# Performance work log

Measured on AMD Instinct MI355X. Metric: run time of the kernel, lower is better.

Reference implementation:

```python
import jax, jax.numpy as jnp
import numpy as np
from jax import lax

START, STOP, NTAGS = 18, 19, 20
NEG = -10000.0
V, E, H, L = 100000, 300, 512, 512  # vocab, embed_dim, per-direction hidden, seq_len


def setup_inputs() -> dict:
    key = jax.random.key(0)
    ks = jax.random.split(key, 16)
    f = lambda k, s: jax.random.normal(k, s, dtype=jnp.float32) * 0.05
    trans = jax.random.normal(ks[14], (NTAGS, NTAGS), dtype=jnp.float32)
    trans = trans.at[START, :].set(NEG).at[:, STOP].set(NEG)
    return {
        "sentence": jax.random.randint(ks[0], (L,), 0, V),
        "embed_table": f(ks[1], (V, E)),
        "w_ih_f": f(ks[2], (4 * H, E)), "w_hh_f": f(ks[3], (4 * H, H)),
        "b_ih_f": f(ks[4], (4 * H,)), "b_hh_f": f(ks[5], (4 * H,)),
        "w_ih_b": f(ks[6], (4 * H, E)), "w_hh_b": f(ks[7], (4 * H, H)),
        "b_ih_b": f(ks[8], (4 * H,)), "b_hh_b": f(ks[9], (4 * H,)),
        "h0": f(ks[10], (2, H)), "c0": f(ks[11], (2, H)),
        "w_out": f(ks[12], (NTAGS, 2 * H)), "b_out": f(ks[13], (NTAGS,)),
        "transitions": trans,
    }


def _lstm_dir(x, wih, whh, bih, bhh, h0, c0, reverse):
    # x: [L, E]; PyTorch gate order i, f, g, o
    b = bih + bhh
    def step(carry, xt):
        h, c = carry
        g = xt @ wih.T + h @ whh.T + b  # [4H]
        i, fg, gg, o = jnp.split(g, 4)
        c = jax.nn.sigmoid(fg) * c + jax.nn.sigmoid(i) * jnp.tanh(gg)
        h = jax.nn.sigmoid(o) * jnp.tanh(c)
        return (h, c), h
    _, hs = lax.scan(step, (h0, c0), x, reverse=reverse)
    return hs  # [L, H] in time order


def _lstm_feats(sentence, embed_table, w_ih_f, w_hh_f, b_ih_f, b_hh_f,
                w_ih_b, w_hh_b, b_ih_b, b_hh_b, h0, c0, w_out, b_out):
    x = embed_table[sentence]  # [L, E]
    hf = _lstm_dir(x, w_ih_f, w_hh_f, b_ih_f, b_hh_f, h0[0], c0[0], False)
    hb = _lstm_dir(x, w_ih_b, w_hh_b, b_ih_b, b_hh_b, h0[1], c0[1], True)
    h = jnp.concatenate([hf, hb], axis=-1)  # [L, 2H]
    return h @ w_out.T + b_out  # [L, NTAGS]


def reference(sentence, embed_table, w_ih_f, w_hh_f, b_ih_f, b_hh_f,
              w_ih_b, w_hh_b, b_ih_b, b_hh_b, h0, c0, w_out, b_out, transitions):
    feats = _lstm_feats(sentence, embed_table, w_ih_f, w_hh_f, b_ih_f, b_hh_f,
                        w_ih_b, w_hh_b, b_ih_b, b_hh_b, h0, c0, w_out, b_out)
    init = jnp.full((NTAGS,), NEG, dtype=feats.dtype).at[START].set(0.0)

    def vstep(fv, feat):
        scores = fv[None, :] + transitions  # [next_tag, prev_tag]
        bptr = jnp.argmax(scores, axis=1)
        return jnp.max(scores, axis=1) + feat, bptr

    fv, bptrs = lax.scan(vstep, init, feats)  # bptrs: [L, NTAGS]
    terminal = fv + transitions[STOP]
    best = jnp.argmax(terminal)

    def back(tag, bp):
        # tag is the best tag at step t; bp maps tag_t -> tag_{t-1}
        return bp[tag], tag

    _, path = lax.scan(back, best, bptrs, reverse=True)  # [L] in time order
    return path
```

## Files before the change

### kernel.cpp

```cpp
#include <hip/hip_runtime.h>
#include <math.h>

typedef unsigned long long u64;
typedef unsigned int u32;

#define L 512
#define E 300
#define H 512
#define G4H 2048
#define NTAGS 20
#define START_TAG 18
#define STOP_TAG 19

#define KC 100

#define OFF_XW    0u
#define OFF_HIST  8388608u
#define OFF_HBUF  10485760u
#define OFF_FEATS 10502144u

__global__ __launch_bounds__(256) void k1_xw(
    const int* __restrict__ sentence, const float* __restrict__ embed,
    const float* __restrict__ wih_f, const float* __restrict__ wih_b,
    const float* __restrict__ bih_f, const float* __restrict__ bhh_f,
    const float* __restrict__ bih_b, const float* __restrict__ bhh_b,
    float* __restrict__ xw) {
    __shared__ float wST[KC][68];
    __shared__ float xST[KC][68];
    __shared__ int   sT[64];

    const int tid = threadIdx.x;
    const int tx = tid & 15;
    const int ty = tid >> 4;
    const int n_base = blockIdx.x * 64;
    const int t_base = blockIdx.y * 64;
    const int dir = blockIdx.z;
    const float* wih = dir ? wih_b : wih_f;
    const float* bih = dir ? bih_b : bih_f;
    const float* bhh = dir ? bhh_b : bhh_f;

    if (tid < 64) sT[tid] = sentence[t_base + tid];
    __syncthreads();

    float acc[4][4];
#pragma unroll
    for (int i = 0; i < 4; ++i)
#pragma unroll
        for (int j = 0; j < 4; ++j) acc[i][j] = 0.f;

    for (int kc = 0; kc < E; kc += KC) {
#pragma unroll
        for (int i = 0; i < 25; ++i) {
            int idx = i * 256 + tid;
            int row = idx / KC, col = idx % KC;
            wST[col][row] = wih[(size_t)(n_base + row) * E + kc + col];
        }
#pragma unroll
        for (int i = 0; i < 25; ++i) {
            int idx = i * 256 + tid;
            int trow = idx / KC, col = idx % KC;
            xST[col][trow] = embed[(size_t)sT[trow] * E + kc + col];
        }
        __syncthreads();

#pragma unroll 4
        for (int k = 0; k < KC; ++k) {
            float4 wv4 = *(const float4*)&wST[k][ty * 4];
            float4 xv4 = *(const float4*)&xST[k][tx * 4];
            float wv[4] = {wv4.x, wv4.y, wv4.z, wv4.w};
            float xv[4] = {xv4.x, xv4.y, xv4.z, xv4.w};
#pragma unroll
            for (int i = 0; i < 4; ++i)
#pragma unroll
                for (int j = 0; j < 4; ++j)
                    acc[i][j] = fmaf(wv[i], xv[j], acc[i][j]);
        }
        __syncthreads();
    }

#pragma unroll
    for (int i = 0; i < 4; ++i) {
        int n = n_base + ty * 4 + i;
        float b = bih[n] + bhh[n];
        int u = n & (H - 1), g = n >> 9;
        int pos = (u >> 4) * 64 + g * 16 + (u & 15);
#pragma unroll
        for (int j = 0; j < 4; ++j) {
            int t = t_base + tx * 4 + j;
            xw[((size_t)(dir * L) + t) * G4H + pos] = acc[i][j] + b;
        }
    }
}

__global__ __launch_bounds__(512, 1) void k2_lstm(
    const float* __restrict__ whh_f, const float* __restrict__ whh_b,
    const float* __restrict__ h0, const float* __restrict__ c0,
    const float* __restrict__ xw, float* __restrict__ hist,
    u64* __restrict__ hbuf) {
    const int bid = blockIdx.x;
    const int dir = bid >> 5;
    const int wg  = bid & 31;
    const int tid = threadIdx.x;
    const int wv  = tid >> 6;
    const int l   = tid & 63;
    const int g   = l >> 4;
    const int j   = l & 15;
    const int grow = g * H + wg * 16 + j;

    const float* whh = dir ? whh_b : whh_f;
    float* histd = hist + (size_t)dir * L * H;
    u64* hb = hbuf + dir * 1024;

    float w[64];
    {
        const float* wp = whh + (size_t)grow * H + wv * 64;
#pragma unroll
        for (int i = 0; i < 64; i += 4) {
            float4 v = *(const float4*)(wp + i);
            w[i] = v.x; w[i+1] = v.y; w[i+2] = v.z; w[i+3] = v.w;
        }
    }

    __shared__ float pbuf[2][8][68];

    float c = (tid < 16) ? c0[dir * H + wg * 16 + tid] : 0.f;

    for (int s = 1; s <= L; ++s) {
        const int t = dir ? (L - s) : (s - 1);
        const int par = s & 1;

        float xwv = 0.f;
        if (tid < 64)
            xwv = xw[((size_t)(dir * L) + t) * G4H + wg * 64 + l];

        float hval;
        if (s == 1) {
            hval = h0[dir * H + tid];
        } else {
            const u32 want = (u32)(s - 1);
            u64* slot = hb + ((s - 1) & 1) * 512 + tid;
            u64 v0 = __hip_atomic_load(slot, __ATOMIC_RELAXED, __HIP_MEMORY_SCOPE_AGENT);
            u64 v1 = __hip_atomic_load(slot, __ATOMIC_RELAXED, __HIP_MEMORY_SCOPE_AGENT);
            u64 v2 = __hip_atomic_load(slot, __ATOMIC_RELAXED, __HIP_MEMORY_SCOPE_AGENT);
            while ((u32)(v0 >> 32) != want) {
                v0 = v1; v1 = v2;
                v2 = __hip_atomic_load(slot, __ATOMIC_RELAXED, __HIP_MEMORY_SCOPE_AGENT);
            }
            hval = __uint_as_float((u32)v0);
        }

        float a0 = 0.f, a1 = 0.f, a2 = 0.f, a3 = 0.f;
#pragma unroll
        for (int i = 0; i < 64; i += 4) {
            float h0v = __uint_as_float((u32)__builtin_amdgcn_readlane(
                            (int)__float_as_uint(hval), i));
            float h1v = __uint_as_float((u32)__builtin_amdgcn_readlane(
                            (int)__float_as_uint(hval), i + 1));
            float h2v = __uint_as_float((u32)__builtin_amdgcn_readlane(
                            (int)__float_as_uint(hval), i + 2));
            float h3v = __uint_as_float((u32)__builtin_amdgcn_readlane(
                            (int)__float_as_uint(hval), i + 3));
            a0 = fmaf(w[i],     h0v, a0);
            a1 = fmaf(w[i + 1], h1v, a1);
            a2 = fmaf(w[i + 2], h2v, a2);
            a3 = fmaf(w[i + 3], h3v, a3);
        }
        pbuf[par][wv][l] = (a0 + a1) + (a2 + a3);
        __syncthreads();

        if (tid < 64) {
            float tot = 0.f;
#pragma unroll
            for (int p = 0; p < 8; ++p) tot += pbuf[par][p][l];
            float pre = tot + xwv;
            float aa = (g == 2) ? 2.f * pre : pre;
            float sg = 1.f / (1.f + __expf(-aa));
            float vg = (g == 2) ? (2.f * sg - 1.f) : sg;
            float gi = __shfl(vg, j);
            float gf = __shfl(vg, 16 + j);
            float gg = __shfl(vg, 32 + j);
            float go = __shfl(vg, 48 + j);
            if (tid < 16) {
                c = gf * c + gi * gg;
                float th = 2.f / (1.f + __expf(-2.f * c)) - 1.f;
                float hout = go * th;
                u64 e = ((u64)(u32)s << 32) | (u64)__float_as_uint(hout);
                __hip_atomic_store(hb + par * 512 + wg * 16 + tid, e,
                                   __ATOMIC_RELAXED, __HIP_MEMORY_SCOPE_AGENT);
                histd[(size_t)t * H + wg * 16 + tid] = hout;
            }
        }
    }
}

__global__ void k3_feats(const float* __restrict__ hist,
                         const float* __restrict__ wout,
                         const float* __restrict__ bout,
                         float* __restrict__ feats) {
    int t = blockIdx.x;
    int tid = threadIdx.x;
    int tag = tid >> 4;
    int part = tid & 15;
    const float* h0p = hist + (size_t)t * H;
    const float* h1p = hist + (size_t)L * H + (size_t)t * H;
    int j0 = part * 64;
    float acc = 0.f;
    for (int jj = 0; jj < 64; jj += 4) {
        int j = j0 + jj;
        float4 w4 = *(const float4*)(wout + (size_t)tag * (2 * H) + j);
        float4 h4 = (j < H) ? *(const float4*)(h0p + j)
                            : *(const float4*)(h1p + (j - H));
        acc = fmaf(w4.x, h4.x, fmaf(w4.y, h4.y,
              fmaf(w4.z, h4.z, fmaf(w4.w, h4.w, acc))));
    }
    acc += __shfl_xor(acc, 8, 16);
    acc += __shfl_xor(acc, 4, 16);
    acc += __shfl_xor(acc, 2, 16);
    acc += __shfl_xor(acc, 1, 16);
    if (part == 0) feats[(size_t)t * NTAGS + tag] = acc + bout[tag];
}

__global__ void k4_viterbi(const float* __restrict__ feats,
                           const float* __restrict__ trans,
                           int* __restrict__ out) {
    __shared__ unsigned char bp[L * NTAGS];
    int lane = threadIdx.x;
    bool act = lane < NTAGS;

    float trl[NTAGS];
#pragma unroll
    for (int p = 0; p < NTAGS; ++p)
        trl[p] = act ? trans[lane * NTAGS + p] : -1.0e30f;

    float fv = (lane == START_TAG) ? 0.f : -10000.f;
    float nf = act ? feats[lane] : 0.f;

    for (int t = 0; t < L; ++t) {
        float f = nf;
        if (act && t + 1 < L) nf = feats[(size_t)(t + 1) * NTAGS + lane];
        float tv[NTAGS];
        int   ti[NTAGS];
#pragma unroll
        for (int p = 0; p < NTAGS; ++p) {
            tv[p] = __shfl(fv, p) + trl[p];
            ti[p] = p;
        }
#pragma unroll
        for (int p = 0; p < 4; ++p) {
            bool take = (tv[p + 16] > tv[p]) ||
                        (tv[p + 16] == tv[p] && ti[p + 16] < ti[p]);
            if (take) { tv[p] = tv[p + 16]; ti[p] = ti[p + 16]; }
        }
#pragma unroll
        for (int w = 8; w >= 1; w >>= 1)
#pragma unroll
            for (int p = 0; p < 16; ++p) if (p < w) {
                bool take = (tv[p + w] > tv[p]) ||
                            (tv[p + w] == tv[p] && ti[p + w] < ti[p]);
                if (take) { tv[p] = tv[p + w]; ti[p] = ti[p + w]; }
            }
        fv = tv[0] + f;
        if (act) bp[t * NTAGS + lane] = (unsigned char)ti[0];
    }

    float ts = act ? fv + trans[STOP_TAG * NTAGS + lane] : -1.0e30f;
    int bi = lane;
#pragma unroll
    for (int off = 32; off; off >>= 1) {
        float ov = __shfl_down(ts, off);
        int   oi = __shfl_down(bi, off);
        if (ov > ts) { ts = ov; bi = oi; }
    }
    if (lane == 0) {
        int tag = bi;
        out[L - 1] = tag;
        for (int t = L - 1; t >= 1; --t) {
            tag = bp[t * NTAGS + tag];
            out[t - 1] = tag;
        }
    }
}

extern "C" void kernel_launch(void* const* d_in, const int* in_sizes, int n_in,
                              void* d_out, int out_size, void* d_ws, size_t ws_size,
                              hipStream_t stream) {
    const int*   sentence = (const int*)d_in[0];
    const float* embed    = (const float*)d_in[1];
    const float* wih_f    = (const float*)d_in[2];
    const float* whh_f    = (const float*)d_in[3];
    const float* bih_f    = (const float*)d_in[4];
    const float* bhh_f    = (const float*)d_in[5];
    const float* wih_b    = (const float*)d_in[6];
    const float* whh_b    = (const float*)d_in[7];
    const float* bih_b    = (const float*)d_in[8];
    const float* bhh_b    = (const float*)d_in[9];
    const float* h0       = (const float*)d_in[10];
    const float* c0       = (const float*)d_in[11];
    const float* wout     = (const float*)d_in[12];
    const float* bout     = (const float*)d_in[13];
    const float* trans    = (const float*)d_in[14];
    int* out = (int*)d_out;

    char* ws = (char*)d_ws;
    float* xw    = (float*)(ws + OFF_XW);
    float* hist  = (float*)(ws + OFF_HIST);
    float* feats = (float*)(ws + OFF_FEATS);
    u64*   hbuf  = (u64*)(ws + OFF_HBUF);

    k1_xw<<<dim3(32, 8, 2), 256, 0, stream>>>(sentence, embed, wih_f, wih_b,
                                              bih_f, bhh_f, bih_b, bhh_b, xw);
    k2_lstm<<<64, 512, 0, stream>>>(whh_f, whh_b, h0, c0, xw, hist, hbuf);
    k3_feats<<<L, 320, 0, stream>>>(hist, wout, bout, feats);
    k4_viterbi<<<1, 64, 0, stream>>>(feats, trans, out);
}
```

Measured before the change: 1.394 ms.

## Pin LSTM workgroups to two XCDs and spin on an sc0 mirror buffer

The recurrent LSTM kernel now launches 256 workgroups. Each reads its XCD id from a hardware register and claims one of the 64 logical slots only when it lands on XCD 0 or 1; unplaced groups back off and claim leftovers, and surplus groups exit. Each hidden-state exchange is also written to a mirror buffer with sc0 stores and polled with pipelined sc0 inline-asm loads, with the agent-scope slot as fallback, so the cross-workgroup handoff can be served from a closer cache level. A large static shared allocation presumably forces one workgroup per CU. The risks are the overhead of extra launched blocks, reuse of the feats region for the mirror and counters, and reliance on cache coherence behaviour of sc0 across CUs.

```diff
diff --git a/kernel.cpp b/kernel.cpp
--- a/kernel.cpp
+++ b/kernel.cpp
@@ -18,6 +18,15 @@
 #define OFF_HIST  8388608u
 #define OFF_HBUF  10485760u
 #define OFF_FEATS 10502144u
+
+__global__ void k0_init(u64* __restrict__ z) {
+    int t = threadIdx.x;
+#pragma unroll
+    for (int i = 0; i < 9; ++i) {
+        int idx = t * 9 + i;
+        if (idx < 2304) z[idx] = 0;
+    }
+}
 
 __global__ __launch_bounds__(256) void k1_xw(
     const int* __restrict__ sentence, const float* __restrict__ embed,
@@ -92,15 +101,51 @@
     }
 }
 
+#define SHM_U64 10800
+
 __global__ __launch_bounds__(512, 1) void k2_lstm(
     const float* __restrict__ whh_f, const float* __restrict__ whh_b,
     const float* __restrict__ h0, const float* __restrict__ c0,
     const float* __restrict__ xw, float* __restrict__ hist,
-    u64* __restrict__ hbuf) {
-    const int bid = blockIdx.x;
-    const int dir = bid >> 5;
-    const int wg  = bid & 31;
+    u64* __restrict__ hbuf, u64* __restrict__ mir,
+    int* __restrict__ cntX, int* __restrict__ claimed) {
+
+    __shared__ u64 shm[SHM_U64];
+    float* pbuf = (float*)(shm + 8);
+#define PB(p, w, l) pbuf[(((p) * 8 + (w)) * 68) + (l)]
+    __shared__ int slot_sh;
+
     const int tid = threadIdx.x;
+
+    if (tid == 0) {
+        shm[SHM_U64 - 1] = 0;
+        u32 xcd = __builtin_amdgcn_s_getreg(14356) & 7;
+        int r = atomicAdd(&cntX[xcd], 1);
+        int slot = -1;
+        if (xcd <= 1 && r < 32) {
+            int cand = (int)xcd * 32 + r;
+            if (atomicCAS(&claimed[cand], 0, 1) == 0) slot = cand;
+        }
+        slot_sh = slot;
+    }
+    __syncthreads();
+    int slot = slot_sh;
+
+    if (slot < 0) {
+        if (tid == 0) {
+            for (int i = 0; i < 8; ++i) __builtin_amdgcn_s_sleep(127);
+            int got = -1;
+            for (int sl = 0; sl < 64 && got < 0; ++sl)
+                if (atomicCAS(&claimed[sl], 0, 1) == 0) got = sl;
+            slot_sh = got;
+        }
+        __syncthreads();
+        slot = slot_sh;
+        if (slot < 0) return;
+    }
+
+    const int dir = slot >> 5;
+    const int wg  = slot & 31;
     const int wv  = tid >> 6;
     const int l   = tid & 63;
     const int g   = l >> 4;
@@ -109,7 +154,8 @@
 
     const float* whh = dir ? whh_b : whh_f;
     float* histd = hist + (size_t)dir * L * H;
-    u64* hb = hbuf + dir * 1024;
+    u64* hb   = hbuf + dir * 1024;
+    u64* mird = mir  + dir * 1024;
 
     float w[64];
     {
@@ -121,33 +167,45 @@
         }
     }
 
-    __shared__ float pbuf[2][8][68];
-
     float c = (tid < 16) ? c0[dir * H + wg * 16 + tid] : 0.f;
 
     for (int s = 1; s <= L; ++s) {
         const int t = dir ? (L - s) : (s - 1);
         const int par = s & 1;
-
-        float xwv = 0.f;
-        if (tid < 64)
-            xwv = xw[((size_t)(dir * L) + t) * G4H + wg * 64 + l];
 
         float hval;
         if (s == 1) {
             hval = h0[dir * H + tid];
         } else {
             const u32 want = (u32)(s - 1);
-            u64* slot = hb + ((s - 1) & 1) * 512 + tid;
-            u64 v0 = __hip_atomic_load(slot, __ATOMIC_RELAXED, __HIP_MEMORY_SCOPE_AGENT);
-            u64 v1 = __hip_atomic_load(slot, __ATOMIC_RELAXED, __HIP_MEMORY_SCOPE_AGENT);
-            u64 v2 = __hip_atomic_load(slot, __ATOMIC_RELAXED, __HIP_MEMORY_SCOPE_AGENT);
-            while ((u32)(v0 >> 32) != want) {
-                v0 = v1; v1 = v2;
-                v2 = __hip_atomic_load(slot, __ATOMIC_RELAXED, __HIP_MEMORY_SCOPE_AGENT);
+            const u64* mslot = mird + ((s - 1) & 1) * 512 + tid;
+            u64* cslot = hb + ((s - 1) & 1) * 512 + tid;
+            u64 va, vb, got;
+            asm volatile("global_load_dwordx2 %0, %2, off sc0\n\t"
+                         "global_load_dwordx2 %1, %2, off sc0"
+                         : "=&v"(va), "=&v"(vb)
+                         : "v"(mslot) : "memory");
+            while (true) {
+                asm volatile("s_waitcnt vmcnt(1)" : "+v"(va) :: "memory");
+                __builtin_amdgcn_sched_barrier(0);
+                if ((u32)(va >> 32) == want) { got = va; break; }
+                asm volatile("global_load_dwordx2 %0, %1, off sc0"
+                             : "=&v"(va) : "v"(mslot) : "memory");
+                asm volatile("s_waitcnt vmcnt(1)" : "+v"(vb) :: "memory");
+                __builtin_amdgcn_sched_barrier(0);
+                if ((u32)(vb >> 32) == want) { got = vb; break; }
+                asm volatile("global_load_dwordx2 %0, %1, off sc0"
+                             : "=&v"(vb) : "v"(mslot) : "memory");
+                u64 vc = __hip_atomic_load(cslot, __ATOMIC_RELAXED,
+                                           __HIP_MEMORY_SCOPE_AGENT);
+                if ((u32)(vc >> 32) == want) { got = vc; break; }
             }
-            hval = __uint_as_float((u32)v0);
-        }
+            hval = __uint_as_float((u32)got);
+        }
+
+        float xwv = 0.f;
+        if (tid < 64)
+            xwv = xw[((size_t)(dir * L) + t) * G4H + wg * 64 + l];
 
         float a0 = 0.f, a1 = 0.f, a2 = 0.f, a3 = 0.f;
 #pragma unroll
@@ -165,13 +223,13 @@
             a2 = fmaf(w[i + 2], h2v, a2);
             a3 = fmaf(w[i + 3], h3v, a3);
         }
-        pbuf[par][wv][l] = (a0 + a1) + (a2 + a3);
+        PB(par, wv, l) = (a0 + a1) + (a2 + a3);
         __syncthreads();
 
         if (tid < 64) {
             float tot = 0.f;
 #pragma unroll
-            for (int p = 0; p < 8; ++p) tot += pbuf[par][p][l];
+            for (int p = 0; p < 8; ++p) tot += PB(par, p, l);
             float pre = tot + xwv;
             float aa = (g == 2) ? 2.f * pre : pre;
             float sg = 1.f / (1.f + __expf(-aa));
@@ -185,12 +243,16 @@
                 float th = 2.f / (1.f + __expf(-2.f * c)) - 1.f;
                 float hout = go * th;
                 u64 e = ((u64)(u32)s << 32) | (u64)__float_as_uint(hout);
+                const u64* ma = mird + par * 512 + wg * 16 + tid;
+                asm volatile("global_store_dwordx2 %0, %1, off sc0"
+                             :: "v"(ma), "v"(e) : "memory");
                 __hip_atomic_store(hb + par * 512 + wg * 16 + tid, e,
                                    __ATOMIC_RELAXED, __HIP_MEMORY_SCOPE_AGENT);
                 histd[(size_t)t * H + wg * 16 + tid] = hout;
             }
         }
     }
+#undef PB
 }
 
 __global__ void k3_feats(const float* __restrict__ hist,
@@ -306,10 +368,15 @@
     float* hist  = (float*)(ws + OFF_HIST);
     float* feats = (float*)(ws + OFF_FEATS);
     u64*   hbuf  = (u64*)(ws + OFF_HBUF);
-
+    u64*   mir   = (u64*)(ws + OFF_FEATS);
+    int*   cntX  = (int*)(ws + OFF_FEATS + 16384);
+    int*   claimed = cntX + 8;
+
+    k0_init<<<1, 256, 0, stream>>>(mir);
     k1_xw<<<dim3(32, 8, 2), 256, 0, stream>>>(sentence, embed, wih_f, wih_b,
                                               bih_f, bhh_f, bih_b, bhh_b, xw);
-    k2_lstm<<<64, 512, 0, stream>>>(whh_f, whh_b, h0, c0, xw, hist, hbuf);
+    k2_lstm<<<256, 512, 0, stream>>>(whh_f, whh_b, h0, c0, xw, hist, hbuf,
+                                     mir, cntX, claimed);
     k3_feats<<<L, 320, 0, stream>>>(hist, wout, bout, feats);
     k4_viterbi<<<1, 64, 0, stream>>>(feats, trans, out);
 }
```

Result: no change. 1.400 ms (+0.4%).
